# Optimization experiments

Hardware: AMD Instinct MI355X
Metric: run time of the kernel (lower is better)

## Reference

```python
import jax, jax.numpy as jnp
import numpy as np

INPUT_DIM = 256
HIDDEN_DIM = 1024
OUTPUT_DIM = 128
BATCH = 128
SEQ_LEN = 1024


def setup_inputs() -> dict:
    key = jax.random.key(0)
    ks = jax.random.split(key, 7)
    s_ih = 1.0 / np.sqrt(HIDDEN_DIM)
    return {
        "sequence": jax.random.normal(ks[0], (BATCH, SEQ_LEN, INPUT_DIM), dtype=jnp.float32),
        # nn.LSTMCell params: gates ordered (i, f, g, o), W_ih: [4H, D], W_hh: [4H, H]
        "W_ih": jax.random.uniform(ks[1], (4 * HIDDEN_DIM, INPUT_DIM), jnp.float32, -s_ih, s_ih),
        "W_hh": jax.random.uniform(ks[2], (4 * HIDDEN_DIM, HIDDEN_DIM), jnp.float32, -s_ih, s_ih),
        "b_ih": jax.random.uniform(ks[3], (4 * HIDDEN_DIM,), jnp.float32, -s_ih, s_ih),
        "b_hh": jax.random.uniform(ks[4], (4 * HIDDEN_DIM,), jnp.float32, -s_ih, s_ih),
        # nn.Linear(hidden_dim, output_dim)
        "W_out": jax.random.uniform(ks[5], (OUTPUT_DIM, HIDDEN_DIM), jnp.float32, -s_ih, s_ih),
        "b_out": jax.random.uniform(ks[6], (OUTPUT_DIM,), jnp.float32, -s_ih, s_ih),
    }


def reference(sequence, W_ih, W_hh, b_ih, b_hh, W_out, b_out):
    B = sequence.shape[0]
    H = W_hh.shape[1]
    dtype = sequence.dtype

    def step(carry, x_t):
        hx, cx = carry
        # LSTMCell: gates = x W_ih^T + b_ih + h W_hh^T + b_hh, split as (i, f, g, o)
        gates = x_t @ W_ih.T + b_ih + hx @ W_hh.T + b_hh  # [B, 4H]
        i, f, g, o = jnp.split(gates, 4, axis=-1)
        i = jax.nn.sigmoid(i)
        f = jax.nn.sigmoid(f)
        g = jnp.tanh(g)
        o = jax.nn.sigmoid(o)
        cx = f * cx + i * g
        hx = o * jnp.tanh(cx)
        # dropout p=0.0 -> identity; per-step head + log-softmax
        out = jax.nn.log_softmax(hx @ W_out.T + b_out, axis=-1)  # [B, V]
        return (hx, cx), out

    # forward loops over timesteps 0..T-2
    xs = jnp.swapaxes(sequence[:, :-1, :], 0, 1)  # [T-1, B, D]
    init = (jnp.zeros((B, H), dtype), jnp.zeros((B, H), dtype))
    _, outs = jax.lax.scan(step, init, xs)  # [T-1, B, V]
    return jnp.swapaxes(outs, 0, 1)  # [B, T-1, V]
```

## Files before the change

### kernel.cpp

```cpp
#include <hip/hip_runtime.h>

#define T_SEQ   1024
#define T_STEPS 1023
#define BATCH   128
#define DIM     256
#define HID     1024
#define VOUT    128
#define WGS     256
#define HSLOT   131072
#define SLICE_E 16384
#define XSLICE  4096

typedef __attribute__((ext_vector_type(8))) short short8;
typedef __attribute__((ext_vector_type(4))) float floatx4;

#define GLDS(gp, lp) __builtin_amdgcn_global_load_lds( \
    (const __attribute__((address_space(1))) unsigned int*)(gp), \
    (__attribute__((address_space(3))) unsigned int*)(lp), 16, 0, 0)

__device__ __forceinline__ unsigned short f2bf(float x) {
    union { float f; unsigned u; } v; v.f = x;
    unsigned r = v.u + 0x7FFFu + ((v.u >> 16) & 1u);
    return (unsigned short)(r >> 16);
}
__device__ __forceinline__ float sigm(float x) { return 1.0f / (1.0f + __expf(-x)); }


__global__ void pack_w(const float* __restrict__ Whh, unsigned short* __restrict__ Wph) {
    const size_t idx = (size_t)blockIdx.x * 256 + threadIdx.x;
    if (idx >= (size_t)32 * 8 * 32 * 64 * 8) return;
    const int j   = (int)(idx & 7);
    const int l   = (int)((idx >> 3) & 63);
    const int rest = (int)(idx >> 9);
    const int i2  = rest & 31;
    const int w   = (rest >> 5) & 7;
    const int cg  = rest >> 8;
    const int tile = i2 >> 3, hi = i2 & 7;
    const int cw = w >> 2, kw = w & 3;
    const int gc = cw * 64 + tile * 16 + (l & 15);
    const int R  = (gc >> 5) * HID + cg * 32 + (gc & 31);
    const int hcol = (kw * 8 + hi) * 32 + (l >> 4) * 8 + j;
    Wph[idx] = f2bf(Whh[(size_t)R * HID + hcol]);
}

__global__ void pack_xw(const float* __restrict__ Wih, unsigned short* __restrict__ Xw) {
    const size_t idx = (size_t)blockIdx.x * 256 + threadIdx.x;
    if (idx >= (size_t)32 * 8 * 8 * 64 * 8) return;
    const int j   = (int)(idx & 7);
    const int l   = (int)((idx >> 3) & 63);
    const int rest = (int)(idx >> 9);
    const int fi  = rest & 7;
    const int w   = (rest >> 3) & 7;
    const int cg  = rest >> 6;
    const int tile = fi >> 1, xi = fi & 1;
    const int cw = w >> 2, kw = w & 3;
    const int gc = cw * 64 + tile * 16 + (l & 15);
    const int R  = (gc >> 5) * HID + cg * 32 + (gc & 31);
    const int xcol = (kw * 2 + xi) * 32 + (l >> 4) * 8 + j;
    Xw[idx] = f2bf(Wih[(size_t)R * DIM + xcol]);
}

__global__ void pack_bias(const float* __restrict__ bih, const float* __restrict__ bhh,
                          float* __restrict__ bc) {
    const int idx = blockIdx.x * 256 + threadIdx.x;
    if (idx < 4096) bc[idx] = bih[idx] + bhh[idx];
}

__global__ void pack_wout(const float* __restrict__ Wo, unsigned short* __restrict__ WoBf) {
    const int idx = blockIdx.x * 256 + threadIdx.x;
    if (idx < VOUT * HID) WoBf[idx] = f2bf(Wo[idx]);
}

__global__ void pack_x(const float* __restrict__ seq, unsigned short* __restrict__ Xb) {
    const size_t idx = (size_t)blockIdx.x * 256 + threadIdx.x;
    if (idx >= (size_t)T_STEPS * BATCH * DIM) return;
    const int j   = (int)(idx & 7);
    const int row = (int)((idx >> 3) & 15);
    const int lq  = (int)((idx >> 7) & 3);
    const int kk  = (int)((idx >> 9) & 7);
    const int s8  = (int)((idx >> 12) & 7);
    const int t   = (int)(idx >> 15);
    const int b = s8 * 16 + row;
    const int k = kk * 32 + lq * 8 + j;
    Xb[idx] = f2bf(seq[((size_t)b * T_SEQ + t) * DIM + k]);
}

__global__ void init_state(unsigned short* __restrict__ Hb, int* __restrict__ bar) {
    const int idx = blockIdx.x * 256 + threadIdx.x;
    if (idx < HSLOT) Hb[idx] = 0;
    if (idx < 4096) bar[idx] = 0;
}

__global__ __launch_bounds__(512, 1) void lstm_persist(
    const unsigned short* __restrict__ Xb,
    unsigned short* __restrict__ Hblk,
    const unsigned short* __restrict__ Wph,
    const unsigned short* __restrict__ Xw,
    const float* __restrict__ bc,
    int* __restrict__ bar)
{
    __shared__ short8 xwl[64 * 64];
    __shared__ float  gl[4][16][132];

    const int wg  = blockIdx.x;
    const int s8  = wg & 7;
    const int cg  = wg >> 3;
    const int tid = threadIdx.x;
    const int w   = tid >> 6;
    const int l   = tid & 63;
    const int lr  = l & 15;
    const int lq  = l >> 4;
    const int cw  = w >> 2;
    const int kw  = w & 3;
    const int cbase = cw * 64;
    const int lq4 = lq * 4;

    {
        const unsigned short* xsrc = Xw + (size_t)cg * 32768;
        #pragma unroll
        for (int i = 0; i < 8; ++i)
            GLDS(xsrc + i * 4096 + tid * 8, (unsigned short*)xwl + i * 4096 + tid * 8);
    }

    const short8* wpw = (const short8*)Wph + (size_t)(cg * 8 + w) * 32 * 64 + l;
    short8 bh[32];
    #pragma unroll
    for (int i = 0; i < 32; ++i) bh[i] = wpw[i * 64];

    const int er  = (tid >> 3) & 15;
    const int ej  = tid & 7;
    const int elq = tid >> 7;
    const int hc  = elq * 8 + ej;
    const float bi  = bc[0 * HID + cg * 32 + hc];
    const float bf_ = bc[1 * HID + cg * 32 + hc];
    const float bg  = bc[2 * HID + cg * 32 + hc];
    const float bo_ = bc[3 * HID + cg * 32 + hc];
    float creg = 0.f;

    __syncthreads();

    const short8* xwv = xwl + (w * 8) * 64 + l;
    const unsigned short* hb0 = Hblk + (size_t)s8 * SLICE_E + (size_t)(kw * 8) * 512 + (size_t)l * 8;
    const unsigned short* xa0 = Xb + (size_t)s8 * XSLICE + (size_t)(kw * 2) * 512 + (size_t)l * 8;
    int* flagp = &bar[s8 * 64 + kw * 8 + (l & 7)];

    floatx4 acx0 = {0.f,0.f,0.f,0.f}, acx1 = acx0, acx2 = acx0, acx3 = acx0;
    #pragma unroll
    for (int xi = 0; xi < 2; ++xi) {
        short8 a = *(const short8*)(xa0 + xi * 512);
        acx0 = __builtin_amdgcn_mfma_f32_16x16x32_bf16(a, xwv[(0*2+xi)*64], acx0, 0,0,0);
        acx1 = __builtin_amdgcn_mfma_f32_16x16x32_bf16(a, xwv[(1*2+xi)*64], acx1, 0,0,0);
        acx2 = __builtin_amdgcn_mfma_f32_16x16x32_bf16(a, xwv[(2*2+xi)*64], acx2, 0,0,0);
        acx3 = __builtin_amdgcn_mfma_f32_16x16x32_bf16(a, xwv[(3*2+xi)*64], acx3, 0,0,0);
    }

    for (int t = 0; t < T_STEPS; ++t) {
        #pragma unroll
        for (int i = 0; i < 32; ++i) asm volatile("" : "+v"(bh[i]));

        {
            const unsigned short* hp = hb0 + (size_t)t * HSLOT;
            short8 ha[8];
            #pragma unroll
            for (int i = 0; i < 8; ++i) ha[i] = *(const short8*)(hp + i * 512);
            #pragma unroll
            for (int i = 0; i < 8; ++i) {
                acx0 = __builtin_amdgcn_mfma_f32_16x16x32_bf16(ha[i], bh[ 0 + i], acx0, 0,0,0);
                acx1 = __builtin_amdgcn_mfma_f32_16x16x32_bf16(ha[i], bh[ 8 + i], acx1, 0,0,0);
                acx2 = __builtin_amdgcn_mfma_f32_16x16x32_bf16(ha[i], bh[16 + i], acx2, 0,0,0);
                acx3 = __builtin_amdgcn_mfma_f32_16x16x32_bf16(ha[i], bh[24 + i], acx3, 0,0,0);
            }
        }

        #pragma unroll
        for (int r = 0; r < 4; ++r) {
            gl[kw][lq4 + r][cbase      + lr] = acx0[r];
            gl[kw][lq4 + r][cbase + 16 + lr] = acx1[r];
            gl[kw][lq4 + r][cbase + 32 + lr] = acx2[r];
            gl[kw][lq4 + r][cbase + 48 + lr] = acx3[r];
        }
        __syncthreads();

        float gi = bi, gf = bf_, gg = bg, go = bo_;
        #pragma unroll
        for (int q = 0; q < 4; ++q) {
            gi += gl[q][er][ 0 + hc];
            gf += gl[q][er][32 + hc];
            gg += gl[q][er][64 + hc];
            go += gl[q][er][96 + hc];
        }
        const float iv = sigm(gi), fv = sigm(gf), ov = sigm(go);
        const float gv = tanhf(gg);
        creg = fv * creg + iv * gv;
        const unsigned hu = f2bf(ov * tanhf(creg));
        const unsigned up = (unsigned)__shfl_down((int)hu, 1);
        if ((tid & 1) == 0) {
            unsigned* hp = (unsigned*)(Hblk + (size_t)(t + 1) * HSLOT
                          + (size_t)s8 * SLICE_E + (size_t)cg * 512 + tid);
            __hip_atomic_store(hp, hu | (up << 16), __ATOMIC_RELAXED, __HIP_MEMORY_SCOPE_AGENT);
        }
        __syncthreads();

        if (t + 1 < T_STEPS) {
            if (tid == 0)
                __hip_atomic_store(&bar[s8 * 64 + cg], t + 1,
                                   __ATOMIC_RELAXED, __HIP_MEMORY_SCOPE_AGENT);

            const unsigned short* xp = xa0 + (size_t)(t + 1) * (BATCH * DIM);
            const floatx4 z = {0.f, 0.f, 0.f, 0.f};
            acx0 = z; acx1 = z; acx2 = z; acx3 = z;
            #pragma unroll
            for (int xi = 0; xi < 2; ++xi) {
                short8 a = *(const short8*)(xp + xi * 512);
                acx0 = __builtin_amdgcn_mfma_f32_16x16x32_bf16(a, xwv[(0*2+xi)*64], acx0, 0,0,0);
                acx1 = __builtin_amdgcn_mfma_f32_16x16x32_bf16(a, xwv[(1*2+xi)*64], acx1, 0,0,0);
                acx2 = __builtin_amdgcn_mfma_f32_16x16x32_bf16(a, xwv[(2*2+xi)*64], acx2, 0,0,0);
                acx3 = __builtin_amdgcn_mfma_f32_16x16x32_bf16(a, xwv[(3*2+xi)*64], acx3, 0,0,0);
            }

            {
                const int need = t + 1;
                int bud = 1 << 22;
                while (true) {
                    const int f = __hip_atomic_load(flagp, __ATOMIC_RELAXED,
                                                    __HIP_MEMORY_SCOPE_AGENT);
                    if (__all(f >= need)) break;
                    if (--bud < 0) break;
                }
                __builtin_amdgcn_sched_barrier(0);
            }
        }
    }
}

__global__ __launch_bounds__(256, 2) void head_ls(
    const unsigned short* __restrict__ Hblk,
    const unsigned short* __restrict__ Wo,
    const float* __restrict__ bo,
    float* __restrict__ out)
{
    const int bg = blockIdx.x;
    const int t  = blockIdx.y;
    const int tid = threadIdx.x;
    const int w  = tid >> 6;
    const int l  = tid & 63;
    const int lr = l & 15;
    const int lq = l >> 4;
    const int b0 = bg * 16;

    const short8* ap = (const short8*)(Hblk + (size_t)(t + 1) * HSLOT
                       + (size_t)bg * SLICE_E) + l;
    const unsigned short* bp0 = Wo + (size_t)(w * 32 + lr) * HID + lq * 8;
    const unsigned short* bp1 = Wo + (size_t)(w * 32 + 16 + lr) * HID + lq * 8;

    floatx4 a0 = {0.f, 0.f, 0.f, 0.f}, a1 = {0.f, 0.f, 0.f, 0.f};
    #pragma unroll 8
    for (int kk = 0; kk < 32; ++kk) {
        short8 a   = ap[kk * 64];
        short8 b0v = *(const short8*)(bp0 + kk * 32);
        short8 b1v = *(const short8*)(bp1 + kk * 32);
        a0 = __builtin_amdgcn_mfma_f32_16x16x32_bf16(a, b0v, a0, 0, 0, 0);
        a1 = __builtin_amdgcn_mfma_f32_16x16x32_bf16(a, b1v, a1, 0, 0, 0);
    }

    __shared__ float lg[16][132];
    #pragma unroll
    for (int r = 0; r < 4; ++r) {
        lg[lq * 4 + r][w * 32 + lr]      = a0[r] + bo[w * 32 + lr];
        lg[lq * 4 + r][w * 32 + 16 + lr] = a1[r] + bo[w * 32 + 16 + lr];
    }
    __syncthreads();

    const int row = tid >> 4;
    const int c   = tid & 15;
    float vals[8];
    float m = -1e30f;
    #pragma unroll
    for (int jv = 0; jv < 8; ++jv) { vals[jv] = lg[row][c + jv * 16]; m = fmaxf(m, vals[jv]); }
    #pragma unroll
    for (int d = 8; d >= 1; d >>= 1) m = fmaxf(m, __shfl_xor(m, d, 16));
    float ssum = 0.f;
    #pragma unroll
    for (int jv = 0; jv < 8; ++jv) ssum += __expf(vals[jv] - m);
    #pragma unroll
    for (int d = 8; d >= 1; d >>= 1) ssum += __shfl_xor(ssum, d, 16);
    const float lse = m + __logf(ssum);

    float* op = out + ((size_t)(b0 + row) * T_STEPS + t) * VOUT;
    #pragma unroll
    for (int jv = 0; jv < 8; ++jv) op[c + jv * 16] = vals[jv] - lse;
}

extern "C" void kernel_launch(void* const* d_in, const int* in_sizes, int n_in,
                              void* d_out, int out_size, void* d_ws, size_t ws_size,
                              hipStream_t stream) {
    const float* seq  = (const float*)d_in[0];
    const float* Wih  = (const float*)d_in[1];
    const float* Whh  = (const float*)d_in[2];
    const float* bih  = (const float*)d_in[3];
    const float* bhh  = (const float*)d_in[4];
    const float* Wout = (const float*)d_in[5];
    const float* bout = (const float*)d_in[6];
    float* out = (float*)d_out;

    char* p = (char*)d_ws;
    unsigned short* Wph  = (unsigned short*)p; p += (size_t)32 * 8 * 32 * 64 * 8 * 2;
    unsigned short* Xw   = (unsigned short*)p; p += (size_t)32 * 8 * 8 * 64 * 8 * 2;
    unsigned short* WoBf = (unsigned short*)p; p += (size_t)VOUT * HID * 2;
    float*          bc   = (float*)p;          p += (size_t)4096 * 4;
    int*            bar  = (int*)p;            p += (size_t)4096 * 4;
    unsigned short* Xb   = (unsigned short*)p; p += (size_t)T_STEPS * BATCH * DIM * 2;
    unsigned short* Hblk = (unsigned short*)p; p += (size_t)(T_STEPS + 1) * HSLOT * 2;

    pack_w    <<<16384, 256, 0, stream>>>(Whh, Wph);
    pack_xw   <<<4096,  256, 0, stream>>>(Wih, Xw);
    pack_bias <<<16,    256, 0, stream>>>(bih, bhh, bc);
    pack_wout <<<512,   256, 0, stream>>>(Wout, WoBf);
    pack_x    <<<130944,256, 0, stream>>>(seq, Xb);
    init_state<<<512,   256, 0, stream>>>(Hblk, bar);

    lstm_persist<<<WGS, 512, 0, stream>>>(Xb, Hblk, Wph, Xw, bc, bar);

    head_ls<<<dim3(8, T_STEPS), 256, 0, stream>>>(Hblk, WoBf, bout, out);
}
```

Before: 3.631 ms.

## Give each wave full-K gate columns and stage hidden state in LDS

Repacks W_hh and W_ih so each wave owns 4 hidden units across all four gates and the full K dimension. The cross-wave LDS reduction and its two block barriers become in-register accumulation plus lane shuffles. The hidden-state slice is loaded into LDS with global_load_lds once per step, and a finer per-wave flag scheme replaces the per-block flag. The intent is to shorten the serial per-step critical path, at the cost of more flag polling (4 loads per lane) and a full-block LDS load each step.

```diff
diff --git a/kernel.cpp b/kernel.cpp
--- a/kernel.cpp
+++ b/kernel.cpp
@@ -25,6 +25,18 @@
 }
 __device__ __forceinline__ float sigm(float x) { return 1.0f / (1.0f + __expf(-x)); }
 
+__device__ __forceinline__ floatx4 shflx4(floatx4 v, int mask) {
+    floatx4 r;
+    #pragma unroll
+    for (int i = 0; i < 4; ++i) r[i] = __shfl_xor(v[i], mask, 64);
+    return r;
+}
+__device__ __forceinline__ float sel4(floatx4 v, int s) {
+    const float v01 = (s & 1) ? v[1] : v[0];
+    const float v23 = (s & 1) ? v[3] : v[2];
+    return (s & 2) ? v23 : v01;
+}
+
 
 __global__ void pack_w(const float* __restrict__ Whh, unsigned short* __restrict__ Wph) {
     const size_t idx = (size_t)blockIdx.x * 256 + threadIdx.x;
@@ -32,15 +44,14 @@
     const int j   = (int)(idx & 7);
     const int l   = (int)((idx >> 3) & 63);
     const int rest = (int)(idx >> 9);
-    const int i2  = rest & 31;
+    const int hk  = rest & 31;
     const int w   = (rest >> 5) & 7;
     const int cg  = rest >> 8;
-    const int tile = i2 >> 3, hi = i2 & 7;
-    const int cw = w >> 2, kw = w & 3;
-    const int gc = cw * 64 + tile * 16 + (l & 15);
-    const int R  = (gc >> 5) * HID + cg * 32 + (gc & 31);
-    const int hcol = (kw * 8 + hi) * 32 + (l >> 4) * 8 + j;
-    Wph[idx] = f2bf(Whh[(size_t)R * HID + hcol]);
+    const int c = l & 15;
+    const int gate = c >> 2, p = c & 3;
+    const int R = gate * HID + cg * 32 + w * 4 + p;
+    const int kcol = hk * 32 + (l >> 4) * 8 + j;
+    Wph[idx] = f2bf(Whh[(size_t)R * HID + kcol]);
 }
 
 __global__ void pack_xw(const float* __restrict__ Wih, unsigned short* __restrict__ Xw) {
@@ -49,15 +60,14 @@
     const int j   = (int)(idx & 7);
     const int l   = (int)((idx >> 3) & 63);
     const int rest = (int)(idx >> 9);
-    const int fi  = rest & 7;
+    const int xk  = rest & 7;
     const int w   = (rest >> 3) & 7;
     const int cg  = rest >> 6;
-    const int tile = fi >> 1, xi = fi & 1;
-    const int cw = w >> 2, kw = w & 3;
-    const int gc = cw * 64 + tile * 16 + (l & 15);
-    const int R  = (gc >> 5) * HID + cg * 32 + (gc & 31);
-    const int xcol = (kw * 2 + xi) * 32 + (l >> 4) * 8 + j;
-    Xw[idx] = f2bf(Wih[(size_t)R * DIM + xcol]);
+    const int c = l & 15;
+    const int gate = c >> 2, p = c & 3;
+    const int R = gate * HID + cg * 32 + w * 4 + p;
+    const int kcol = xk * 32 + (l >> 4) * 8 + j;
+    Xw[idx] = f2bf(Wih[(size_t)R * DIM + kcol]);
 }
 
 __global__ void pack_bias(const float* __restrict__ bih, const float* __restrict__ bhh,
@@ -99,8 +109,8 @@
     const float* __restrict__ bc,
     int* __restrict__ bar)
 {
-    __shared__ short8 xwl[64 * 64];
-    __shared__ float  gl[4][16][132];
+    __shared__ short8 xwl[4096];
+    __shared__ short8 hl[2048];
 
     const int wg  = blockIdx.x;
     const int s8  = wg & 7;
@@ -108,12 +118,10 @@
     const int tid = threadIdx.x;
     const int w   = tid >> 6;
     const int l   = tid & 63;
-    const int lr  = l & 15;
-    const int lq  = l >> 4;
-    const int cw  = w >> 2;
-    const int kw  = w & 3;
-    const int cbase = cw * 64;
-    const int lq4 = lq * 4;
+    const int c   = l & 15;
+    const int q   = l >> 4;
+    const int gate = c >> 2;
+    const int p    = c & 3;
 
     {
         const unsigned short* xsrc = Xw + (size_t)cg * 32768;
@@ -127,107 +135,113 @@
     #pragma unroll
     for (int i = 0; i < 32; ++i) bh[i] = wpw[i * 64];
 
-    const int er  = (tid >> 3) & 15;
-    const int ej  = tid & 7;
-    const int elq = tid >> 7;
-    const int hc  = elq * 8 + ej;
-    const float bi  = bc[0 * HID + cg * 32 + hc];
-    const float bf_ = bc[1 * HID + cg * 32 + hc];
-    const float bg  = bc[2 * HID + cg * 32 + hc];
-    const float bo_ = bc[3 * HID + cg * 32 + hc];
+    const float bcol = bc[gate * HID + cg * 32 + w * 4 + p];
     float creg = 0.f;
 
     __syncthreads();
 
     const short8* xwv = xwl + (w * 8) * 64 + l;
-    const unsigned short* hb0 = Hblk + (size_t)s8 * SLICE_E + (size_t)(kw * 8) * 512 + (size_t)l * 8;
-    const unsigned short* xa0 = Xb + (size_t)s8 * XSLICE + (size_t)(kw * 2) * 512 + (size_t)l * 8;
-    int* flagp = &bar[s8 * 64 + kw * 8 + (l & 7)];
-
-    floatx4 acx0 = {0.f,0.f,0.f,0.f}, acx1 = acx0, acx2 = acx0, acx3 = acx0;
-    #pragma unroll
-    for (int xi = 0; xi < 2; ++xi) {
-        short8 a = *(const short8*)(xa0 + xi * 512);
-        acx0 = __builtin_amdgcn_mfma_f32_16x16x32_bf16(a, xwv[(0*2+xi)*64], acx0, 0,0,0);
-        acx1 = __builtin_amdgcn_mfma_f32_16x16x32_bf16(a, xwv[(1*2+xi)*64], acx1, 0,0,0);
-        acx2 = __builtin_amdgcn_mfma_f32_16x16x32_bf16(a, xwv[(2*2+xi)*64], acx2, 0,0,0);
-        acx3 = __builtin_amdgcn_mfma_f32_16x16x32_bf16(a, xwv[(3*2+xi)*64], acx3, 0,0,0);
-    }
+    const short8* hv  = hl + l;
+    const unsigned short* xa0 = Xb + (size_t)s8 * XSLICE + (size_t)l * 8;
+    int* flagme = &bar[s8 * 256 + cg * 8 + w];
+    const int* fb = bar + s8 * 256 + l * 4;
+
+    const floatx4 z = {0.f, 0.f, 0.f, 0.f};
+    floatx4 aA = z, aB = z, aC = z, aD = z;
+
+    #pragma unroll
+    for (int xk = 0; xk < 8; xk += 2) {
+        short8 a0v = *(const short8*)(xa0 + xk * 512);
+        short8 a1v = *(const short8*)(xa0 + (xk + 1) * 512);
+        aA = __builtin_amdgcn_mfma_f32_16x16x32_bf16(a0v, xwv[xk * 64],       aA, 0, 0, 0);
+        aB = __builtin_amdgcn_mfma_f32_16x16x32_bf16(a1v, xwv[(xk + 1) * 64], aB, 0, 0, 0);
+    }
+
+    long bud = 1L << 22;
 
     for (int t = 0; t < T_STEPS; ++t) {
-        #pragma unroll
-        for (int i = 0; i < 32; ++i) asm volatile("" : "+v"(bh[i]));
+        while (true) {
+            const int f0 = __hip_atomic_load(fb + 0, __ATOMIC_RELAXED, __HIP_MEMORY_SCOPE_AGENT);
+            const int f1 = __hip_atomic_load(fb + 1, __ATOMIC_RELAXED, __HIP_MEMORY_SCOPE_AGENT);
+            const int f2 = __hip_atomic_load(fb + 2, __ATOMIC_RELAXED, __HIP_MEMORY_SCOPE_AGENT);
+            const int f3 = __hip_atomic_load(fb + 3, __ATOMIC_RELAXED, __HIP_MEMORY_SCOPE_AGENT);
+            const int mn = min(min(f0, f1), min(f2, f3));
+            if (__all(mn >= t)) break;
+            if (--bud < 0) break;
+        }
+        asm volatile("" ::: "memory");
+        __builtin_amdgcn_sched_barrier(0);
 
         {
-            const unsigned short* hp = hb0 + (size_t)t * HSLOT;
-            short8 ha[8];
+            const unsigned short* hs = Hblk + (size_t)t * HSLOT + (size_t)s8 * SLICE_E;
             #pragma unroll
-            for (int i = 0; i < 8; ++i) ha[i] = *(const short8*)(hp + i * 512);
+            for (int i = 0; i < 4; ++i)
+                GLDS(hs + i * 4096 + tid * 8, (unsigned short*)hl + i * 4096 + tid * 8);
+        }
+        __syncthreads();
+
+        #pragma unroll
+        for (int f = 0; f < 32; f += 4) {
+            short8 h0 = hv[(f + 0) * 64];
+            short8 h1 = hv[(f + 1) * 64];
+            short8 h2 = hv[(f + 2) * 64];
+            short8 h3 = hv[(f + 3) * 64];
+            aA = __builtin_amdgcn_mfma_f32_16x16x32_bf16(h0, bh[f + 0], aA, 0, 0, 0);
+            aB = __builtin_amdgcn_mfma_f32_16x16x32_bf16(h1, bh[f + 1], aB, 0, 0, 0);
+            aC = __builtin_amdgcn_mfma_f32_16x16x32_bf16(h2, bh[f + 2], aC, 0, 0, 0);
+            aD = __builtin_amdgcn_mfma_f32_16x16x32_bf16(h3, bh[f + 3], aD, 0, 0, 0);
+        }
+        floatx4 acc = (aA + aB) + (aC + aD);
+        #pragma unroll
+        for (int r = 0; r < 4; ++r) acc[r] += bcol;
+
+        const floatx4 t1 = shflx4(acc, 4);
+        floatx4 ev, od;
+        #pragma unroll
+        for (int r = 0; r < 4; ++r) {
+            ev[r] = (gate & 1) ? t1[r] : acc[r];
+            od[r] = (gate & 1) ? acc[r] : t1[r];
+        }
+        const floatx4 t2 = shflx4(ev, 8);
+        const floatx4 t3 = shflx4(od, 8);
+        floatx4 gI, gF, gG, gO;
+        #pragma unroll
+        for (int r = 0; r < 4; ++r) {
+            gI[r] = (gate & 2) ? t2[r] : ev[r];
+            gG[r] = (gate & 2) ? ev[r] : t2[r];
+            gF[r] = (gate & 2) ? t3[r] : od[r];
+            gO[r] = (gate & 2) ? od[r] : t3[r];
+        }
+
+        const float iv = sigm(sel4(gI, gate));
+        const float fv = sigm(sel4(gF, gate));
+        const float gv = tanhf(sel4(gG, gate));
+        const float ov = sigm(sel4(gO, gate));
+        creg = fv * creg + iv * gv;
+        const unsigned hu = (unsigned)f2bf(ov * tanhf(creg));
+        const unsigned hup = (unsigned)__shfl_xor((int)hu, 1, 64);
+
+        if ((c & 1) == 0) {
+            const int row = q * 4 + gate;
+            unsigned* hp = (unsigned*)(Hblk + (size_t)(t + 1) * HSLOT
+                          + (size_t)s8 * SLICE_E + (size_t)cg * 512)
+                          + ((w >> 1) * 64 + row * 4 + (w & 1) * 2 + (p >> 1));
+            __hip_atomic_store(hp, hu | (hup << 16), __ATOMIC_RELAXED, __HIP_MEMORY_SCOPE_AGENT);
+        }
+        asm volatile("s_waitcnt vmcnt(0)" ::: "memory");
+
+        aA = z; aB = z; aC = z; aD = z;
+        if (t + 1 < T_STEPS) {
+            if (l == 0)
+                __hip_atomic_store(flagme, t + 1, __ATOMIC_RELAXED, __HIP_MEMORY_SCOPE_AGENT);
+
+            const unsigned short* xp = xa0 + (size_t)(t + 1) * (BATCH * DIM);
             #pragma unroll
-            for (int i = 0; i < 8; ++i) {
-                acx0 = __builtin_amdgcn_mfma_f32_16x16x32_bf16(ha[i], bh[ 0 + i], acx0, 0,0,0);
-                acx1 = __builtin_amdgcn_mfma_f32_16x16x32_bf16(ha[i], bh[ 8 + i], acx1, 0,0,0);
-                acx2 = __builtin_amdgcn_mfma_f32_16x16x32_bf16(ha[i], bh[16 + i], acx2, 0,0,0);
-                acx3 = __builtin_amdgcn_mfma_f32_16x16x32_bf16(ha[i], bh[24 + i], acx3, 0,0,0);
-            }
-        }
-
-        #pragma unroll
-        for (int r = 0; r < 4; ++r) {
-            gl[kw][lq4 + r][cbase      + lr] = acx0[r];
-            gl[kw][lq4 + r][cbase + 16 + lr] = acx1[r];
-            gl[kw][lq4 + r][cbase + 32 + lr] = acx2[r];
-            gl[kw][lq4 + r][cbase + 48 + lr] = acx3[r];
-        }
-        __syncthreads();
-
-        float gi = bi, gf = bf_, gg = bg, go = bo_;
-        #pragma unroll
-        for (int q = 0; q < 4; ++q) {
-            gi += gl[q][er][ 0 + hc];
-            gf += gl[q][er][32 + hc];
-            gg += gl[q][er][64 + hc];
-            go += gl[q][er][96 + hc];
-        }
-        const float iv = sigm(gi), fv = sigm(gf), ov = sigm(go);
-        const float gv = tanhf(gg);
-        creg = fv * creg + iv * gv;
-        const unsigned hu = f2bf(ov * tanhf(creg));
-        const unsigned up = (unsigned)__shfl_down((int)hu, 1);
-        if ((tid & 1) == 0) {
-            unsigned* hp = (unsigned*)(Hblk + (size_t)(t + 1) * HSLOT
-                          + (size_t)s8 * SLICE_E + (size_t)cg * 512 + tid);
-            __hip_atomic_store(hp, hu | (up << 16), __ATOMIC_RELAXED, __HIP_MEMORY_SCOPE_AGENT);
-        }
-        __syncthreads();
-
-        if (t + 1 < T_STEPS) {
-            if (tid == 0)
-                __hip_atomic_store(&bar[s8 * 64 + cg], t + 1,
-                                   __ATOMIC_RELAXED, __HIP_MEMORY_SCOPE_AGENT);
-
-            const unsigned short* xp = xa0 + (size_t)(t + 1) * (BATCH * DIM);
-            const floatx4 z = {0.f, 0.f, 0.f, 0.f};
-            acx0 = z; acx1 = z; acx2 = z; acx3 = z;
-            #pragma unroll
-            for (int xi = 0; xi < 2; ++xi) {
-                short8 a = *(const short8*)(xp + xi * 512);
-                acx0 = __builtin_amdgcn_mfma_f32_16x16x32_bf16(a, xwv[(0*2+xi)*64], acx0, 0,0,0);
-                acx1 = __builtin_amdgcn_mfma_f32_16x16x32_bf16(a, xwv[(1*2+xi)*64], acx1, 0,0,0);
-                acx2 = __builtin_amdgcn_mfma_f32_16x16x32_bf16(a, xwv[(2*2+xi)*64], acx2, 0,0,0);
-                acx3 = __builtin_amdgcn_mfma_f32_16x16x32_bf16(a, xwv[(3*2+xi)*64], acx3, 0,0,0);
-            }
-
-            {
-                const int need = t + 1;
-                int bud = 1 << 22;
-                while (true) {
-                    const int f = __hip_atomic_load(flagp, __ATOMIC_RELAXED,
-                                                    __HIP_MEMORY_SCOPE_AGENT);
-                    if (__all(f >= need)) break;
-                    if (--bud < 0) break;
-                }
-                __builtin_amdgcn_sched_barrier(0);
+            for (int xk = 0; xk < 8; xk += 2) {
+                short8 a0v = *(const short8*)(xp + xk * 512);
+                short8 a1v = *(const short8*)(xp + (xk + 1) * 512);
+                aA = __builtin_amdgcn_mfma_f32_16x16x32_bf16(a0v, xwv[xk * 64],       aA, 0, 0, 0);
+                aB = __builtin_amdgcn_mfma_f32_16x16x32_bf16(a1v, xwv[(xk + 1) * 64], aB, 0, 0, 0);
             }
         }
     }
@@ -272,11 +286,11 @@
     __syncthreads();
 
     const int row = tid >> 4;
-    const int c   = tid & 15;
+    const int cc  = tid & 15;
     float vals[8];
     float m = -1e30f;
     #pragma unroll
-    for (int jv = 0; jv < 8; ++jv) { vals[jv] = lg[row][c + jv * 16]; m = fmaxf(m, vals[jv]); }
+    for (int jv = 0; jv < 8; ++jv) { vals[jv] = lg[row][cc + jv * 16]; m = fmaxf(m, vals[jv]); }
     #pragma unroll
     for (int d = 8; d >= 1; d >>= 1) m = fmaxf(m, __shfl_xor(m, d, 16));
     float ssum = 0.f;
@@ -288,7 +302,7 @@
 
     float* op = out + ((size_t)(b0 + row) * T_STEPS + t) * VOUT;
     #pragma unroll
-    for (int jv = 0; jv < 8; ++jv) op[c + jv * 16] = vals[jv] - lse;
+    for (int jv = 0; jv < 8; ++jv) op[cc + jv * 16] = vals[jv] - lse;
 }
 
 extern "C" void kernel_launch(void* const* d_in, const int* in_sizes, int n_in,
```

New measurement: 4.517 ms. 1.24x slower.

## Assign LSTM workgroups by hardware XCD ID to keep batch slices chiplet-local

Applied to the files above, without the earlier changes.

Each workgroup now reads its XCC_ID hardware register and takes a rank from an atomic counter, so it derives its batch slice (s8) and column group (cg) from the chiplet it actually runs on rather than from blockIdx. The intent is that all workgroups exchanging hidden state for one batch slice share an XCD and its L2, which cuts cross-chiplet traffic on the per-step barrier and the h-state reads. The flag layout changes to 32 per slice, the flag wait moves to the top of each step, and plain stores followed by an explicit vmcnt wait replace the atomic stores for h. This relies on exactly 32 workgroups landing on each XCD; any other distribution breaks the mapping and correctness, and the bounded spin loop can exit silently on timeout.

```diff
diff --git a/kernel.cpp b/kernel.cpp
--- a/kernel.cpp
+++ b/kernel.cpp
@@ -101,10 +101,8 @@
 {
     __shared__ short8 xwl[64 * 64];
     __shared__ float  gl[4][16][132];
-
-    const int wg  = blockIdx.x;
-    const int s8  = wg & 7;
-    const int cg  = wg >> 3;
+    __shared__ int sreg[2];
+
     const int tid = threadIdx.x;
     const int w   = tid >> 6;
     const int l   = tid & 63;
@@ -115,6 +113,19 @@
     const int cbase = cw * 64;
     const int lq4 = lq * 4;
 
+    if (tid == 0) {
+        int xcd;
+        asm volatile("s_getreg_b32 %0, hwreg(HW_REG_XCC_ID)" : "=s"(xcd));
+        xcd &= 7;
+        const int rank = __hip_atomic_fetch_add(&bar[384 + xcd], 1,
+                             __ATOMIC_RELAXED, __HIP_MEMORY_SCOPE_AGENT);
+        sreg[0] = xcd;
+        sreg[1] = rank & 31;
+    }
+    __syncthreads();
+    const int s8 = sreg[0];
+    const int cg = sreg[1];
+
     {
         const unsigned short* xsrc = Xw + (size_t)cg * 32768;
         #pragma unroll
@@ -142,7 +153,8 @@
     const short8* xwv = xwl + (w * 8) * 64 + l;
     const unsigned short* hb0 = Hblk + (size_t)s8 * SLICE_E + (size_t)(kw * 8) * 512 + (size_t)l * 8;
     const unsigned short* xa0 = Xb + (size_t)s8 * XSLICE + (size_t)(kw * 2) * 512 + (size_t)l * 8;
-    int* flagp = &bar[s8 * 64 + kw * 8 + (l & 7)];
+    const int* fpoll = bar + s8 * 32 + (l & 31);
+    int* flagme = bar + s8 * 32 + cg;
 
     floatx4 acx0 = {0.f,0.f,0.f,0.f}, acx1 = acx0, acx2 = acx0, acx3 = acx0;
     #pragma unroll
@@ -154,9 +166,17 @@
         acx3 = __builtin_amdgcn_mfma_f32_16x16x32_bf16(a, xwv[(3*2+xi)*64], acx3, 0,0,0);
     }
 
+    long bud = 1L << 22;
+
     for (int t = 0; t < T_STEPS; ++t) {
-        #pragma unroll
-        for (int i = 0; i < 32; ++i) asm volatile("" : "+v"(bh[i]));
+        while (true) {
+            const int f = __hip_atomic_load(fpoll, __ATOMIC_RELAXED,
+                                            __HIP_MEMORY_SCOPE_AGENT);
+            if (__all(f >= t)) break;
+            if (--bud < 0) break;
+        }
+        asm volatile("" ::: "memory");
+        __builtin_amdgcn_sched_barrier(0);
 
         {
             const unsigned short* hp = hb0 + (size_t)t * HSLOT;
@@ -194,16 +214,18 @@
         creg = fv * creg + iv * gv;
         const unsigned hu = f2bf(ov * tanhf(creg));
         const unsigned up = (unsigned)__shfl_down((int)hu, 1);
+
         if ((tid & 1) == 0) {
             unsigned* hp = (unsigned*)(Hblk + (size_t)(t + 1) * HSLOT
                           + (size_t)s8 * SLICE_E + (size_t)cg * 512 + tid);
-            __hip_atomic_store(hp, hu | (up << 16), __ATOMIC_RELAXED, __HIP_MEMORY_SCOPE_AGENT);
-        }
+            *hp = hu | (up << 16);
+        }
+        asm volatile("s_waitcnt vmcnt(0)" ::: "memory");
         __syncthreads();
 
         if (t + 1 < T_STEPS) {
             if (tid == 0)
-                __hip_atomic_store(&bar[s8 * 64 + cg], t + 1,
+                __hip_atomic_store(flagme, t + 1,
                                    __ATOMIC_RELAXED, __HIP_MEMORY_SCOPE_AGENT);
 
             const unsigned short* xp = xa0 + (size_t)(t + 1) * (BATCH * DIM);
@@ -216,18 +238,6 @@
                 acx1 = __builtin_amdgcn_mfma_f32_16x16x32_bf16(a, xwv[(1*2+xi)*64], acx1, 0,0,0);
                 acx2 = __builtin_amdgcn_mfma_f32_16x16x32_bf16(a, xwv[(2*2+xi)*64], acx2, 0,0,0);
                 acx3 = __builtin_amdgcn_mfma_f32_16x16x32_bf16(a, xwv[(3*2+xi)*64], acx3, 0,0,0);
-            }
-
-            {
-                const int need = t + 1;
-                int bud = 1 << 22;
-                while (true) {
-                    const int f = __hip_atomic_load(flagp, __ATOMIC_RELAXED,
-                                                    __HIP_MEMORY_SCOPE_AGENT);
-                    if (__all(f >= need)) break;
-                    if (--bud < 0) break;
-                }
-                __builtin_amdgcn_sched_barrier(0);
             }
         }
     }
```

New measurement: 4.367 ms. 1.2x slower.
